# Performance work log

Measured on AMD Instinct MI355X. Metric: run time of the kernel, lower is better.

Reference implementation:

```python
import jax, jax.numpy as jnp
import numpy as np

B, N, C, K = 4, 4096, 64, 16
EPS = 1e-5


def _bn(x, g, b, m, v):
    # eval-mode BatchNorm2d on [B, C, N, K]
    scale = (g / jnp.sqrt(v + EPS))[None, :, None, None]
    return (x - m[None, :, None, None]) * scale + b[None, :, None, None]


def setup_inputs() -> dict:
    key = jax.random.key(0)
    ks = jax.random.split(key, 32)
    s = 0.05
    inp = {
        "p": jax.random.normal(ks[0], (B, N, 3), jnp.float32),
        "x": jax.random.normal(ks[1], (B, C, N), jnp.float32),
        "mask": jnp.ones((B, N), dtype=bool),
        # q/k/v 1x1 Conv1d weights [out, in] + bias
        "Wq": jax.random.normal(ks[2], (C, C)) * s, "bq": jax.random.normal(ks[3], (C,)) * s,
        "Wk": jax.random.normal(ks[4], (C, C)) * s, "bk": jax.random.normal(ks[5], (C,)) * s,
        "Wv": jax.random.normal(ks[6], (C, C)) * s, "bv": jax.random.normal(ks[7], (C,)) * s,
        # pos-enc: Conv2d(3->C, no bias), BN, ReLU, Conv2d(C->C)
        "pe_w1": jax.random.normal(ks[8], (C, 3)) * s,
        "pe_bn_g": jax.random.normal(ks[9], (C,)) * s + 1.0,
        "pe_bn_b": jax.random.normal(ks[10], (C,)) * s,
        "pe_bn_m": jax.random.normal(ks[11], (C,)) * s,
        "pe_bn_v": jax.random.uniform(ks[12], (C,), minval=0.5, maxval=1.5),
        "pe_w2": jax.random.normal(ks[13], (C, C)) * s, "pe_b2": jax.random.normal(ks[14], (C,)) * s,
        # attn: BN, ReLU, Conv2d(C->C, no bias), BN, ReLU, Conv2d(C->C)
        "at_bn0_g": jax.random.normal(ks[15], (C,)) * s + 1.0,
        "at_bn0_b": jax.random.normal(ks[16], (C,)) * s,
        "at_bn0_m": jax.random.normal(ks[17], (C,)) * s,
        "at_bn0_v": jax.random.uniform(ks[18], (C,), minval=0.5, maxval=1.5),
        "at_w1": jax.random.normal(ks[19], (C, C)) * s,
        "at_bn1_g": jax.random.normal(ks[20], (C,)) * s + 1.0,
        "at_bn1_b": jax.random.normal(ks[21], (C,)) * s,
        "at_bn1_m": jax.random.normal(ks[22], (C,)) * s,
        "at_bn1_v": jax.random.uniform(ks[23], (C,), minval=0.5, maxval=1.5),
        "at_w2": jax.random.normal(ks[24], (C, C)) * s, "at_b2": jax.random.normal(ks[25], (C,)) * s,
    }
    return inp


def reference(p, x, mask, Wq, bq, Wk, bk, Wv, bv,
              pe_w1, pe_bn_g, pe_bn_b, pe_bn_m, pe_bn_v, pe_w2, pe_b2,
              at_bn0_g, at_bn0_b, at_bn0_m, at_bn0_v, at_w1,
              at_bn1_g, at_bn1_b, at_bn1_m, at_bn1_v, at_w2, at_b2):
    # q, k, v: 1x1 Conv1d -> [B, C, N]
    q = jnp.einsum('oc,bcn->bon', Wq, x) + bq[None, :, None]
    k = jnp.einsum('oc,bcn->bon', Wk, x) + bk[None, :, None]
    v = jnp.einsum('oc,bcn->bon', Wv, x) + bv[None, :, None]

    # ---- knn_point(K, p, p): Euclidean cdist, zero-point masking, topk smallest
    sq = jnp.sum(p * p, axis=-1)                                   # [B, N]
    d2 = sq[:, :, None] + sq[:, None, :] - 2.0 * jnp.einsum('bnc,bmc->bnm', p, p)
    dist = jnp.sqrt(jnp.maximum(d2, 0.0))                          # [B, N, N]
    valid = ~jnp.all(p == 0, axis=-1)                              # [B, N]
    dist = jnp.where(valid[:, None, :], dist, jnp.inf)
    _, idx = jax.lax.top_k(-dist, K)                               # [B, N, K]

    gather = jax.vmap(lambda a, i: a[i])                           # ([N,C],[N,K]) -> [N,K,C]
    n_k = gather(jnp.transpose(k, (0, 2, 1)), idx)                 # [B, N, K, C]
    n_v = gather(jnp.transpose(v, (0, 2, 1)), idx)                 # [B, N, K, C]
    n_p = gather(p, idx)                                           # [B, N, K, 3]

    rel = p[:, :, None, :] - n_p                                   # [B, N, K, 3]
    rel = jnp.transpose(rel, (0, 3, 1, 2))                         # [B, 3, N, K]

    # position encoding MLP
    h = jnp.einsum('oc,bcnk->bonk', pe_w1, rel)
    h = jax.nn.relu(_bn(h, pe_bn_g, pe_bn_b, pe_bn_m, pe_bn_v))
    n_r = jnp.einsum('oc,bcnk->bonk', pe_w2, h) + pe_b2[None, :, None, None]  # [B,C,N,K]

    # attention MLP on (q - n_k + n_r)
    a = q[:, :, :, None] - jnp.transpose(n_k, (0, 3, 1, 2)) + n_r
    a = jax.nn.relu(_bn(a, at_bn0_g, at_bn0_b, at_bn0_m, at_bn0_v))
    a = jnp.einsum('oc,bcnk->bonk', at_w1, a)
    a = jax.nn.relu(_bn(a, at_bn1_g, at_bn1_b, at_bn1_m, at_bn1_v))
    a = jnp.einsum('oc,bcnk->bonk', at_w2, a) + at_b2[None, :, None, None]

    # mask [B,N] broadcast to [B,C,N,K] (masks query rows, as in original)
    a = jnp.where(mask[:, None, :, None], a, -1e10)
    a = jax.nn.softmax(a, axis=-1)
    a = jnp.where(jnp.isnan(a), 0.0, a)

    y = jnp.sum(a * (jnp.transpose(n_v, (0, 3, 1, 2)) + n_r), axis=-1)  # [B, C, N]
    return (p, y)
```

## Files before the change

### kernel.cpp

```cpp
#include <hip/hip_runtime.h>
#include <stdint.h>

#define NB 4
#define NP 4096
#define NC 64
#define NK 16
#define BN_EPS 1e-5f

typedef __attribute__((ext_vector_type(8))) short short8;
typedef __attribute__((ext_vector_type(4))) float f32x4;
typedef unsigned long long u64;

__device__ __forceinline__ short f2bf(float f) {
    unsigned u = __float_as_uint(f);
    unsigned r = (u + 0x7FFFu + ((u >> 16) & 1u)) >> 16;
    return (short)(unsigned short)r;
}

__global__ __launch_bounds__(256) void px_kernel(const float* __restrict__ p,
                                                 float4* __restrict__ px,
                                                 float* __restrict__ pcopy) {
    int gid = blockIdx.x * 256 + threadIdx.x;
    float x = p[gid * 3 + 0], y = p[gid * 3 + 1], z = p[gid * 3 + 2];
    pcopy[gid * 3 + 0] = x; pcopy[gid * 3 + 1] = y; pcopy[gid * 3 + 2] = z;
    float sq = fmaf(z, z, fmaf(y, y, x * x));
    bool inv = (x == 0.0f) && (y == 0.0f) && (z == 0.0f);
    px[gid] = make_float4(x, y, z, inv ? __builtin_inff() : sq);
}

#define KQW 4
#define KCAP 64

__global__ __launch_bounds__(256) void prep_kernel(
        const float4* __restrict__ px, int* __restrict__ idxout,
        const float* __restrict__ x,
        const float* __restrict__ Wq, const float* __restrict__ bq,
        const float* __restrict__ Wk, const float* __restrict__ bk,
        const float* __restrict__ Wv, const float* __restrict__ bv,
        float* __restrict__ outbase) {
    __shared__ float tb[4][KQW * 64];
    __shared__ u64 sbuf[16][KCAP];
    __shared__ int scnt[16];
    __shared__ float wt[NC * NC];
    __shared__ float bsh[NC];

    if (blockIdx.x < 1024) {
        const int l = threadIdx.x & 63;
        const int w = threadIdx.x >> 6;
        const int gw = blockIdx.x * 4 + w;
        const int q0 = gw * KQW;
        const int b  = q0 >> 12;
        const float4* pb = px + (size_t)b * NP;

        float4 pn[KQW];
#pragma unroll
        for (int j = 0; j < KQW; ++j) pn[j] = px[q0 + j];
        if (l < KQW) scnt[w * KQW + l] = 0;
        __builtin_amdgcn_wave_barrier();

        float k1[KQW];
#pragma unroll
        for (int j = 0; j < KQW; ++j) k1[j] = __builtin_inff();
#pragma unroll 4
        for (int i = 0; i < NP / 64; ++i) {
            float4 pm = pb[i * 64 + l];
#pragma unroll
            for (int j = 0; j < KQW; ++j) {
                float dot = fmaf(pm.z, pn[j].z, fmaf(pm.y, pn[j].y, pm.x * pn[j].x));
                float d2 = fmaxf((pn[j].w + pm.w) - 2.0f * dot, 0.0f);
                k1[j] = fminf(k1[j], d2);
            }
        }
#pragma unroll
        for (int j = 0; j < KQW; ++j) tb[w][j * 64 + l] = k1[j];
        __builtin_amdgcn_wave_barrier();

        float T[KQW];
#pragma unroll
        for (int j = 0; j < KQW; ++j) {
            const float* tj = &tb[w][j * 64];
            int rank = 0;
#pragma unroll 4
            for (int t = 0; t < 64; t += 4) {
                f32x4 v = *(const f32x4*)&tj[t];
                rank += (v[0] < k1[j]) + (v[1] < k1[j]) + (v[2] < k1[j]) + (v[3] < k1[j]);
            }
            float cand = (rank <= 15) ? k1[j] : -__builtin_inff();
#pragma unroll
            for (int off = 32; off; off >>= 1)
                cand = fmaxf(cand, __shfl_xor(cand, off));
            T[j] = cand;
        }

#pragma unroll 2
        for (int i = 0; i < NP / 64; ++i) {
            int m = i * 64 + l;
            float4 pm = pb[m];
#pragma unroll
            for (int j = 0; j < KQW; ++j) {
                float dot = fmaf(pm.z, pn[j].z, fmaf(pm.y, pn[j].y, pm.x * pn[j].x));
                float d2 = fmaxf((pn[j].w + pm.w) - 2.0f * dot, 0.0f);
                if (d2 <= T[j]) {
                    int pos = atomicAdd(&scnt[w * KQW + j], 1);
                    if (pos < KCAP)
                        sbuf[w * KQW + j][pos] =
                            ((u64)__float_as_uint(d2) << 32) | (unsigned int)m;
                }
            }
        }
        __builtin_amdgcn_wave_barrier();

#pragma unroll 1
        for (int j = 0; j < KQW; ++j) {
            int cnt = scnt[w * KQW + j];
            if (cnt > KCAP) cnt = KCAP;
            if (l < cnt) {
                const u64* sb = sbuf[w * KQW + j];
                u64 kj = sb[l];
                int rank = 0;
                for (int t = 0; t < cnt; ++t) rank += (sb[t] < kj);
                if (rank < NK)
                    idxout[(size_t)(q0 + j) * NK + rank] = (int)(kj & 0xffffffffu);
            }
        }
    } else {
        const int qb    = blockIdx.x - 1024;
        const int which = qb >> 8;
        const int bxl   = qb & 255;
        const float* W    = which == 0 ? Wq : which == 1 ? Wk : Wv;
        const float* bias = which == 0 ? bq : which == 1 ? bk : bv;
        float* out = outbase + (size_t)which * NB * NP * NC;

        for (int e = threadIdx.x; e < NC * NC; e += 256)
            wt[(e & 63) * NC + (e >> 6)] = W[e];
        if (threadIdx.x < NC) bsh[threadIdx.x] = bias[threadIdx.x];
        __syncthreads();

        const int gid   = bxl * 256 + threadIdx.x;
        const int token = gid & (NB * NP - 1);
        const int qtr   = gid >> 14;
        const int b = token >> 12, n = token & (NP - 1);

        float acc[16];
#pragma unroll
        for (int o = 0; o < 16; ++o) acc[o] = bsh[qtr * 16 + o];

        const float* xp = x + (size_t)b * NC * NP + n;
#pragma unroll 4
        for (int c = 0; c < NC; ++c) {
            float xc = xp[(size_t)c * NP];
            const float4* wr = (const float4*)&wt[c * NC + qtr * 16];
#pragma unroll
            for (int o4 = 0; o4 < 4; ++o4) {
                float4 w4 = wr[o4];
                acc[o4 * 4 + 0] = fmaf(w4.x, xc, acc[o4 * 4 + 0]);
                acc[o4 * 4 + 1] = fmaf(w4.y, xc, acc[o4 * 4 + 1]);
                acc[o4 * 4 + 2] = fmaf(w4.z, xc, acc[o4 * 4 + 2]);
                acc[o4 * 4 + 3] = fmaf(w4.w, xc, acc[o4 * 4 + 3]);
            }
        }
        float4* op = (float4*)(out + (size_t)token * NC + qtr * 16);
#pragma unroll
        for (int o4 = 0; o4 < 4; ++o4)
            op[o4] = make_float4(acc[o4 * 4 + 0], acc[o4 * 4 + 1],
                                 acc[o4 * 4 + 2], acc[o4 * 4 + 3]);
    }
}

#define QPW 4
#define HBSTR 72

__device__ __forceinline__ short8 pack8(float4 a, float4 b) {
    short8 r;
    r[0] = f2bf(a.x); r[1] = f2bf(a.y); r[2] = f2bf(a.z); r[3] = f2bf(a.w);
    r[4] = f2bf(b.x); r[5] = f2bf(b.y); r[6] = f2bf(b.z); r[7] = f2bf(b.w);
    return r;
}

__device__ __forceinline__ void gemm_stage_lds(const short8 (*__restrict__ WFm)[64],
                                               int l,
                                               const unsigned short* HBw,
                                               float* DBw, int tok, int quad) {
    short8 b0 = *(const short8*)((const char*)HBw + tok * (HBSTR * 2) + quad * 16);
    short8 b1 = *(const short8*)((const char*)HBw + tok * (HBSTR * 2) + 64 + quad * 16);
#pragma unroll
    for (int ob = 0; ob < 4; ++ob) {
        f32x4 acc = {0.0f, 0.0f, 0.0f, 0.0f};
        short8 a0 = WFm[ob * 2 + 0][l];
        short8 a1 = WFm[ob * 2 + 1][l];
        acc = __builtin_amdgcn_mfma_f32_16x16x32_bf16(a0, b0, acc, 0, 0, 0);
        acc = __builtin_amdgcn_mfma_f32_16x16x32_bf16(a1, b1, acc, 0, 0, 0);
#pragma unroll
        for (int r = 0; r < 4; ++r) {
            int row = ob * 16 + quad * 4 + r;
            DBw[tok * 64 + (row ^ tok)] = acc[r];
        }
    }
}

__global__ __launch_bounds__(256, 4) void fused_mfma_kernel(
        const float4* __restrict__ px, const int* __restrict__ idx,
        const float* __restrict__ qT, const float* __restrict__ kT,
        const float* __restrict__ vT,
        const float* __restrict__ pe_w1,
        const float* __restrict__ pe_g, const float* __restrict__ pe_b,
        const float* __restrict__ pe_m, const float* __restrict__ pe_v,
        const float* __restrict__ pe_w2, const float* __restrict__ pe_b2,
        const float* __restrict__ b0g, const float* __restrict__ b0b,
        const float* __restrict__ b0m, const float* __restrict__ b0v,
        const float* __restrict__ at_w1,
        const float* __restrict__ b1g, const float* __restrict__ b1b,
        const float* __restrict__ b1m, const float* __restrict__ b1v,
        const float* __restrict__ at_w2, const float* __restrict__ at_b2,
        float* __restrict__ yout) {
    __shared__ __align__(16) short8 WFl[3][8][64];
    __shared__ __align__(16) float UB[4][16 * 64];

    const int l    = threadIdx.x & 63;
    const int w    = threadIdx.x >> 6;
    const int c    = l;
    const int tok  = l & 15;
    const int quad = l >> 4;

    if (w < 3) {
        const float* Wm = w == 0 ? pe_w2 : w == 1 ? at_w1 : at_w2;
#pragma unroll
        for (int ob = 0; ob < 4; ++ob)
#pragma unroll
            for (int ch = 0; ch < 2; ++ch) {
                const float* src = Wm + (ob * 16 + tok) * NC + ch * 32 + quad * 8;
                float4 a = *(const float4*)src;
                float4 bq4 = *(const float4*)(src + 4);
                WFl[w][ob * 2 + ch][l] = pack8(a, bq4);
            }
    }

    const float pw0 = pe_w1[c * 3 + 0], pw1 = pe_w1[c * 3 + 1], pw2v = pe_w1[c * 3 + 2];
    const float pes = pe_g[c] / sqrtf(pe_v[c] + BN_EPS);
    const float peb = fmaf(-pe_m[c], pes, pe_b[c]);
    const float s0  = b0g[c] / sqrtf(b0v[c] + BN_EPS);
    const float bb0 = fmaf(-b0m[c], s0, b0b[c]);
    const float s1  = b1g[c] / sqrtf(b1v[c] + BN_EPS);
    const float bb1 = fmaf(-b1m[c], s1, b1b[c]);
    const float peb2 = pe_b2[c];
    const float ab2  = at_b2[c];

    __syncthreads();

    unsigned short* HBw = (unsigned short*)UB[w];
    float* DBw = UB[w];

    const int batch = blockIdx.x & 3;
    const int gwb   = (blockIdx.x >> 2) * 4 + w;
    const int q0s   = batch * NP + gwb * QPW;

    for (int jq = 0; jq < QPW; ++jq) {
        const int qi = q0s + jq;
        const int b = qi >> 12, n = qi & (NP - 1);
        const int bNP = b * NP;
        const float4 pn = px[qi];
        const float qv = qT[(size_t)qi * NC + c];

        const int4* ip = (const int4*)(idx + (size_t)qi * NK);
        int4 nid0 = ip[0], nid1 = ip[1], nid2 = ip[2], nid3 = ip[3];
        int mreg[NK];
        mreg[0]  = __builtin_amdgcn_readfirstlane(nid0.x);
        mreg[1]  = __builtin_amdgcn_readfirstlane(nid0.y);
        mreg[2]  = __builtin_amdgcn_readfirstlane(nid0.z);
        mreg[3]  = __builtin_amdgcn_readfirstlane(nid0.w);
        mreg[4]  = __builtin_amdgcn_readfirstlane(nid1.x);
        mreg[5]  = __builtin_amdgcn_readfirstlane(nid1.y);
        mreg[6]  = __builtin_amdgcn_readfirstlane(nid1.z);
        mreg[7]  = __builtin_amdgcn_readfirstlane(nid1.w);
        mreg[8]  = __builtin_amdgcn_readfirstlane(nid2.x);
        mreg[9]  = __builtin_amdgcn_readfirstlane(nid2.y);
        mreg[10] = __builtin_amdgcn_readfirstlane(nid2.z);
        mreg[11] = __builtin_amdgcn_readfirstlane(nid2.w);
        mreg[12] = __builtin_amdgcn_readfirstlane(nid3.x);
        mreg[13] = __builtin_amdgcn_readfirstlane(nid3.y);
        mreg[14] = __builtin_amdgcn_readfirstlane(nid3.z);
        mreg[15] = __builtin_amdgcn_readfirstlane(nid3.w);

        const float4* pxb = px + (size_t)bNP;

#pragma unroll
        for (int h8 = 0; h8 < 2; ++h8) {
            float4 pmr[8];
#pragma unroll
            for (int k = 0; k < 8; ++k) pmr[k] = pxb[mreg[h8 * 8 + k]];
#pragma unroll
            for (int k = 0; k < 8; ++k) {
                float r0 = pn.x - pmr[k].x, r1 = pn.y - pmr[k].y, r2 = pn.z - pmr[k].z;
                float h = fmaf(pw2v, r2, fmaf(pw1, r1, pw0 * r0));
                h = fmaxf(fmaf(h, pes, peb), 0.0f);
                HBw[(h8 * 8 + k) * HBSTR + c] = (unsigned short)f2bf(h);
            }
        }
        __builtin_amdgcn_wave_barrier();

        gemm_stage_lds(WFl[0], l, HBw, DBw, tok, quad);
        __builtin_amdgcn_wave_barrier();

        float nr[NK];
#pragma unroll
        for (int t = 0; t < NK; ++t)
            nr[t] = DBw[t * 64 + (c ^ t)] + peb2;
        __builtin_amdgcn_wave_barrier();

#pragma unroll
        for (int h8 = 0; h8 < 2; ++h8) {
            float kv[8];
#pragma unroll
            for (int k = 0; k < 8; ++k)
                kv[k] = kT[((size_t)(bNP + mreg[h8 * 8 + k])) * NC + c];
#pragma unroll
            for (int k = 0; k < 8; ++k) {
                const int t = h8 * 8 + k;
                float a0 = qv - kv[k] + nr[t];
                a0 = fmaxf(fmaf(a0, s0, bb0), 0.0f);
                HBw[t * HBSTR + c] = (unsigned short)f2bf(a0);
            }
        }
        __builtin_amdgcn_wave_barrier();

        gemm_stage_lds(WFl[1], l, HBw, DBw, tok, quad);
        __builtin_amdgcn_wave_barrier();

        float a1r[NK];
#pragma unroll
        for (int t = 0; t < NK; ++t)
            a1r[t] = DBw[t * 64 + (c ^ t)];
        __builtin_amdgcn_wave_barrier();
#pragma unroll
        for (int t = 0; t < NK; ++t) {
            float a2 = fmaxf(fmaf(a1r[t], s1, bb1), 0.0f);
            HBw[t * HBSTR + c] = (unsigned short)f2bf(a2);
        }
        __builtin_amdgcn_wave_barrier();

        gemm_stage_lds(WFl[2], l, HBw, DBw, tok, quad);
        __builtin_amdgcn_wave_barrier();

        float mxr = -__builtin_inff();
#pragma unroll
        for (int t = 0; t < NK; ++t)
            mxr = fmaxf(mxr, DBw[t * 64 + (c ^ t)]);
        const float mx = mxr + ab2;
        float ssum = 0.0f, yacc = 0.0f;
#pragma unroll
        for (int h8 = 0; h8 < 2; ++h8) {
            float vv[8];
#pragma unroll
            for (int k = 0; k < 8; ++k)
                vv[k] = vT[((size_t)(bNP + mreg[h8 * 8 + k])) * NC + c];
#pragma unroll
            for (int k = 0; k < 8; ++k) {
                const int t = h8 * 8 + k;
                float e = __expf((DBw[t * 64 + (c ^ t)] + ab2) - mx);
                ssum += e;
                yacc = fmaf(e, vv[k] + nr[t], yacc);
            }
        }
        yout[((size_t)(b * NC + c)) * NP + n] = yacc / ssum;
        __builtin_amdgcn_wave_barrier();
    }
}

extern "C" void kernel_launch(void* const* d_in, const int* in_sizes, int n_in,
                              void* d_out, int out_size, void* d_ws, size_t ws_size,
                              hipStream_t stream) {
    const float* p    = (const float*)d_in[0];
    const float* x    = (const float*)d_in[1];
    const float* Wq = (const float*)d_in[3];  const float* bq = (const float*)d_in[4];
    const float* Wk = (const float*)d_in[5];  const float* bk = (const float*)d_in[6];
    const float* Wv = (const float*)d_in[7];  const float* bv = (const float*)d_in[8];
    const float* pe_w1 = (const float*)d_in[9];
    const float* pe_g  = (const float*)d_in[10]; const float* pe_b = (const float*)d_in[11];
    const float* pe_m  = (const float*)d_in[12]; const float* pe_v = (const float*)d_in[13];
    const float* pe_w2 = (const float*)d_in[14]; const float* pe_b2 = (const float*)d_in[15];
    const float* b0g = (const float*)d_in[16]; const float* b0b = (const float*)d_in[17];
    const float* b0m = (const float*)d_in[18]; const float* b0v = (const float*)d_in[19];
    const float* at_w1 = (const float*)d_in[20];
    const float* b1g = (const float*)d_in[21]; const float* b1b = (const float*)d_in[22];
    const float* b1m = (const float*)d_in[23]; const float* b1v = (const float*)d_in[24];
    const float* at_w2 = (const float*)d_in[25]; const float* at_b2 = (const float*)d_in[26];

    const size_t BNC = (size_t)NB * NP * NC;
    float* ws  = (float*)d_ws;
    float* qT  = ws;
    float* kT  = qT + BNC;
    float* vT  = kT + BNC;
    float4* px = (float4*)(vT + BNC);
    int* idx   = (int*)(px + (size_t)NB * NP);

    float* outp = (float*)d_out;
    float* y = outp + (size_t)NB * NP * 3;

    px_kernel<<<dim3(64), dim3(256), 0, stream>>>(p, px, outp);
    prep_kernel<<<dim3(1024 + 768), dim3(256), 0, stream>>>(
        px, idx, x, Wq, bq, Wk, bk, Wv, bv, qT);
    fused_mfma_kernel<<<dim3(1024), dim3(256), 0, stream>>>(
        px, idx, qT, kT, vT, pe_w1, pe_g, pe_b, pe_m, pe_v, pe_w2, pe_b2,
        b0g, b0b, b0m, b0v, at_w1, b1g, b1b, b1m, b1v, at_w2, at_b2, y);
}
```

Measured before the change: 192.8 us.

## Restrict kNN second pass to candidate lanes using ballot-driven compaction

The second distance pass in the kNN selection no longer rescans all points for every query. It only revisits the lanes whose per-lane minimum is within the threshold, since only those lanes can hold selected neighbours. Shared-memory atomics are replaced with wave ballot/popcount compaction, so the count array and its initialisation barrier go away. The ReLU clamp is dropped from the squared distance in the hot loops and applied only when storing. The cost is strided, less coalesced point loads and a data-dependent loop trip count.

```diff
diff --git a/kernel.cpp b/kernel.cpp
--- a/kernel.cpp
+++ b/kernel.cpp
@@ -40,7 +40,6 @@
         float* __restrict__ outbase) {
     __shared__ float tb[4][KQW * 64];
     __shared__ u64 sbuf[16][KCAP];
-    __shared__ int scnt[16];
     __shared__ float wt[NC * NC];
     __shared__ float bsh[NC];
 
@@ -55,8 +54,6 @@
         float4 pn[KQW];
 #pragma unroll
         for (int j = 0; j < KQW; ++j) pn[j] = px[q0 + j];
-        if (l < KQW) scnt[w * KQW + l] = 0;
-        __builtin_amdgcn_wave_barrier();
 
         float k1[KQW];
 #pragma unroll
@@ -67,7 +64,7 @@
 #pragma unroll
             for (int j = 0; j < KQW; ++j) {
                 float dot = fmaf(pm.z, pn[j].z, fmaf(pm.y, pn[j].y, pm.x * pn[j].x));
-                float d2 = fmaxf((pn[j].w + pm.w) - 2.0f * dot, 0.0f);
+                float d2  = fmaf(-2.0f, dot, pn[j].w + pm.w);
                 k1[j] = fminf(k1[j], d2);
             }
         }
@@ -92,33 +89,44 @@
             T[j] = cand;
         }
 
-#pragma unroll 2
-        for (int i = 0; i < NP / 64; ++i) {
-            int m = i * 64 + l;
-            float4 pm = pb[m];
-#pragma unroll
-            for (int j = 0; j < KQW; ++j) {
-                float dot = fmaf(pm.z, pn[j].z, fmaf(pm.y, pn[j].y, pm.x * pn[j].x));
-                float d2 = fmaxf((pn[j].w + pm.w) - 2.0f * dot, 0.0f);
-                if (d2 <= T[j]) {
-                    int pos = atomicAdd(&scnt[w * KQW + j], 1);
-                    if (pos < KCAP)
-                        sbuf[w * KQW + j][pos] =
-                            ((u64)__float_as_uint(d2) << 32) | (unsigned int)m;
-                }
-            }
-        }
-        __builtin_amdgcn_wave_barrier();
-
+        int cnt[KQW];
 #pragma unroll 1
         for (int j = 0; j < KQW; ++j) {
-            int cnt = scnt[w * KQW + j];
-            if (cnt > KCAP) cnt = KCAP;
-            if (l < cnt) {
+            u64 qm = __ballot(k1[j] <= T[j]);
+            int sc = 0;
+            u64* sj = sbuf[w * KQW + j];
+            const float4 pq = pn[j];
+            const float Tj = T[j];
+            while (qm) {
+                int ql = (int)__builtin_ctzll(qm);
+                qm &= qm - 1;
+                float4 pm = pb[l * 64 + ql];
+                float dot = fmaf(pm.z, pq.z, fmaf(pm.y, pq.y, pm.x * pq.x));
+                float d2  = fmaf(-2.0f, dot, pq.w + pm.w);
+                bool sv = (d2 <= Tj);
+                u64 bal = __ballot(sv);
+                if (sv) {
+                    int pos = sc + (int)__popcll(bal & ((1ull << l) - 1ull));
+                    if (pos < KCAP) {
+                        float d2c = fmaxf(d2, 0.0f);
+                        sj[pos] = ((u64)__float_as_uint(d2c) << 32)
+                                  | (unsigned int)(l * 64 + ql);
+                    }
+                }
+                sc += (int)__popcll(bal);
+            }
+            cnt[j] = sc > KCAP ? KCAP : sc;
+        }
+        __builtin_amdgcn_wave_barrier();
+
+#pragma unroll 1
+        for (int j = 0; j < KQW; ++j) {
+            int cj = cnt[j];
+            if (l < cj) {
                 const u64* sb = sbuf[w * KQW + j];
                 u64 kj = sb[l];
                 int rank = 0;
-                for (int t = 0; t < cnt; ++t) rank += (sb[t] < kj);
+                for (int t = 0; t < cj; ++t) rank += (sb[t] < kj);
                 if (rank < NK)
                     idxout[(size_t)(q0 + j) * NK + rank] = (int)(kj & 0xffffffffu);
             }
```

New measurement: 223.7 us. 16.1% more time.
